# Optimization experiments

Measured on AMD Instinct MI355X. Metric: run time of the kernel, lower is better.

Reference implementation:

```python
import jax, jax.numpy as jnp
import numpy as np

NUM_NET = 2
V = 100000
D = 128
B = 4096
K = 5
NS = 10
HYP1 = 0.1
HYP2 = 0.1
HYP3 = 0.1


def setup_inputs() -> dict:
    key = jax.random.key(0)
    ks = jax.random.split(key, 10)
    ri = lambda k, shape: jax.random.randint(k, shape, 0, V, dtype=jnp.int32)
    return {
        "node_tables": jax.random.normal(ks[0], (NUM_NET, V, D), jnp.float32) * 0.1,
        "neigh_tables": jax.random.normal(ks[1], (NUM_NET, V, D), jnp.float32) * 0.1,
        "nodes_idx": ri(ks[2], (NUM_NET, B)),
        "neigh_idx": ri(ks[3], (NUM_NET, B, K)),
        "role_idx": ri(ks[4], (NUM_NET, NUM_NET, B)),
        "neg_main": ri(ks[5], (NUM_NET, B, K * NS)),
        "neg_node": ri(ks[6], (NUM_NET, NUM_NET, B, 1 * NS)),
        "neg_cross": ri(ks[7], (NUM_NET, NUM_NET, B, K * NS)),
        "neg_role": ri(ks[8], (NUM_NET, NUM_NET, B, 1 * NS)),
    }


def _pos_loss(ctx, node):
    # ctx: (B, M, D), node: (B, D) -> mean over all logsigmoid(ctx . node)
    return jax.nn.log_sigmoid(jnp.einsum("bmd,bd->bm", ctx, node)).mean()


def _neg_loss(neg_ctx, node):
    # ctx embeddings are negated: logsigmoid(-(neg . node)), sum over samples, mean over batch
    return jax.nn.log_sigmoid(-jnp.einsum("bmd,bd->bm", neg_ctx, node)).sum(axis=1).mean()


def reference(node_tables, neigh_tables, nodes_idx, neigh_idx, role_idx,
              neg_main, neg_node, neg_cross, neg_role):
    cost = []
    for i in range(NUM_NET):
        node_emb = node_tables[i][nodes_idx[i]]          # (B, D)
        # main SGNS loss on view i (neigh tables)
        neigh_emb = neigh_tables[i][neigh_idx[i]]        # (B, K, D)
        c = _pos_loss(neigh_emb, node_emb) + _neg_loss(neigh_tables[i][neg_main[i]], node_emb)
        cost.append(c)
        # cross-view node alignment (node tables of j at same node indices)
        for j in range(NUM_NET):
            if j != i:
                ctx = node_tables[j][nodes_idx[i]][:, None, :]   # (B, 1, D)
                c = _pos_loss(ctx, node_emb) + _neg_loss(node_tables[j][neg_node[i, j]], node_emb)
                cost.append(HYP1 * c)
        # cross-view neighbor loss (neigh tables of j at view-i neighbor indices)
        for j in range(NUM_NET):
            if j != i:
                ctx = neigh_tables[j][neigh_idx[i]]              # (B, K, D)
                c = _pos_loss(ctx, node_emb) + _neg_loss(neigh_tables[j][neg_cross[i, j]], node_emb)
                cost.append(HYP2 * c)
        # role-based loss (node tables of all j at role indices)
        for j in range(NUM_NET):
            ctx = node_tables[j][role_idx[i, j]][:, None, :]     # (B, 1, D)
            c = _pos_loss(ctx, node_emb) + _neg_loss(node_tables[j][neg_role[i, j]], node_emb)
            cost.append(HYP3 * c)
    total = cost[0]
    for c in cost[1:]:
        total = total + c
    return -total / len(cost)
```

## Files before the change

kernel.cpp:

```cpp
#include <hip/hip_runtime.h>

#define NUM_NET 2
#define V 100000
#define D 128
#define B 4096
#define K 5
#define NS 10

#define W_MAIN_POS (1.0f/20480.0f)
#define W_INV_B    (1.0f/4096.0f)
#define HYP_B      (0.1f/4096.0f)
#define HYP2_BK    (0.1f/20480.0f)

#define GLOBAL_AS __attribute__((address_space(1)))
#define LDS_AS    __attribute__((address_space(3)))

__device__ __forceinline__ void gl_lds16(const float* g, float* l) {
    __builtin_amdgcn_global_load_lds((const GLOBAL_AS unsigned int*)g,
                                     (LDS_AS unsigned int*)l, 16, 0, 0);
}

__device__ __forceinline__ float dot8(float4 a0, float4 a1, float4 b0, float4 b1) {
    return a0.x*b0.x + a0.y*b0.y + a0.z*b0.z + a0.w*b0.w
         + a1.x*b1.x + a1.y*b1.y + a1.z*b1.z + a1.w*b1.w;
}

__device__ __forceinline__ float wlogsig(float pp, int code) {
    float mag = (code == 0) ? W_MAIN_POS
              : (code == 3) ? W_INV_B
              : (code == 6) ? HYP2_BK
              : (code == 7) ? 0.0f
              : HYP_B;
    float x  = (code & 1) ? -pp : pp;
    float ls = fminf(x, 0.0f) - __logf(1.0f + __expf(-fabsf(x)));
    return mag * ls;
}

__global__ __launch_bounds__(256) void rmne_main(
    const float* __restrict__ node_tables,
    const float* __restrict__ neigh_tables,
    const int*   __restrict__ nodes_idx,
    const int*   __restrict__ neigh_idx,
    const int*   __restrict__ role_idx,
    const int*   __restrict__ neg_main,
    const int*   __restrict__ neg_node,
    const int*   __restrict__ neg_cross,
    const int*   __restrict__ neg_role,
    float*       __restrict__ out)
{
    __shared__ float lbuf[4][2][1024];

    const int tid  = threadIdx.x;
    const int lane = tid & 63;
    const int wave = tid >> 6;
    const int unit = blockIdx.x * 4 + wave;
    const int i = unit >> 12;
    const int b = unit & (B - 1);
    const int j = 1 - i;

    int pk[3];
    #pragma unroll
    for (int s = 0; s < 3; ++s) {
        int d = lane + 64 * s;
        int idx = 0, tab = 0, code = 7;
        if      (d <   5) { idx = neigh_idx[(i*B + b)*K + d];              tab = 2 + i; code = 0; }
        else if (d <  55) { idx = neg_main[(i*B + b)*50 + (d-5)];          tab = 2 + i; code = 3; }
        else if (d <  56) { idx = nodes_idx[i*B + b];                      tab = j;     code = 4; }
        else if (d <  66) { idx = neg_node[((i*2+j)*B + b)*NS + (d-56)];   tab = j;     code = 5; }
        else if (d <  71) { idx = neigh_idx[(i*B + b)*K + (d-66)];         tab = 2 + j; code = 6; }
        else if (d < 121) { idx = neg_cross[((i*2+j)*B + b)*50 + (d-71)];  tab = 2 + j; code = 5; }
        else if (d < 122) { idx = role_idx[(i*2+0)*B + b];                 tab = 0;     code = 4; }
        else if (d < 132) { idx = neg_role[((i*2+0)*B + b)*NS + (d-122)];  tab = 0;     code = 5; }
        else if (d < 133) { idx = role_idx[(i*2+1)*B + b];                 tab = 1;     code = 4; }
        else if (d < 143) { idx = neg_role[((i*2+1)*B + b)*NS + (d-133)];  tab = 1;     code = 5; }
        pk[s] = idx | (tab << 20) | (code << 22);
    }

    const int l16     = lane & 15;
    const int quarter = lane >> 4;
    const int nrow    = nodes_idx[i*B + b];
    const float4* nep = (const float4*)(node_tables + ((size_t)i*V + (size_t)nrow)*D) + l16*2;
    const float4 ne0 = nep[0];
    const float4 ne1 = nep[1];

    float acc = 0.0f;

    auto issue = [&](int bb, int parity) {
        float* Lb = &lbuf[wave][parity][0];
        #pragma unroll
        for (int t = 0; t < 4; ++t) {
            int e = 8*bb + 2*t + (lane >> 5);
            int p = __shfl(pk[bb >> 3], e & 63, 64);
            int idx = p & 0xFFFFF;
            int tab = (p >> 20) & 3;
            const float* base = (tab & 2) ? neigh_tables : node_tables;
            const float* g = base + ((size_t)(tab & 1)*V + (size_t)idx)*D + (lane & 31)*4;
            gl_lds16(g, Lb + t*256);
        }
    };

    auto compute = [&](int bb, int parity) {
        const float* Lb = &lbuf[wave][parity][0];
        #pragma unroll
        for (int it = 0; it < 2; ++it) {
            int ein = 4*it + quarter;
            int p = __shfl(pk[bb >> 3], (8*bb + ein) & 63, 64);
            const float4* r = (const float4*)(Lb + ein*128 + l16*8);
            float4 c0 = r[0];
            float4 c1 = r[1];
            float pp = dot8(ne0, ne1, c0, c1);
            pp += __shfl_xor(pp, 1, 64);
            pp += __shfl_xor(pp, 2, 64);
            pp += __shfl_xor(pp, 4, 64);
            pp += __shfl_xor(pp, 8, 64);
            acc += wlogsig(pp, (p >> 22) & 7);
        }
    };

    issue(0, 0);
    #pragma unroll
    for (int bb = 0; bb < 17; ++bb) {
        issue(bb + 1, (bb + 1) & 1);
        asm volatile("s_waitcnt vmcnt(4)" ::: "memory");
        compute(bb, bb & 1);
    }
    asm volatile("s_waitcnt vmcnt(0)" ::: "memory");
    compute(17, 1);

    acc += __shfl_xor(acc, 16, 64);
    acc += __shfl_xor(acc, 32, 64);

    __shared__ float wsum[4];
    if (lane == 0) wsum[wave] = acc;
    __syncthreads();
    if (tid == 0) {
        float s = wsum[0] + wsum[1] + wsum[2] + wsum[3];
        atomicAdd(out, s * (-1.0f / 10.0f));
    }
}

extern "C" void kernel_launch(void* const* d_in, const int* in_sizes, int n_in,
                              void* d_out, int out_size, void* d_ws, size_t ws_size,
                              hipStream_t stream) {
    const float* node_tables  = (const float*)d_in[0];
    const float* neigh_tables = (const float*)d_in[1];
    const int*   nodes_idx    = (const int*)d_in[2];
    const int*   neigh_idx    = (const int*)d_in[3];
    const int*   role_idx     = (const int*)d_in[4];
    const int*   neg_main     = (const int*)d_in[5];
    const int*   neg_node     = (const int*)d_in[6];
    const int*   neg_cross    = (const int*)d_in[7];
    const int*   neg_role     = (const int*)d_in[8];
    float* out = (float*)d_out;

    hipMemsetAsync(out, 0, sizeof(float), stream);
    rmne_main<<<2048, 256, 0, stream>>>(node_tables, neigh_tables, nodes_idx, neigh_idx,
                                        role_idx, neg_main, neg_node, neg_cross, neg_role, out);
}
```

Before: 295.3 us.

## Replace LDS async gather pipeline with register-prefetched direct row loads

Drops the global_load_lds double-buffered staging through shared memory. Each 16-lane quarter now loads its gathered row slice straight into registers through a three-deep rotating prefetch, with 4 rows per step. This removes the LDS writes and reads and the manual vmcnt waits. In exchange it issues extra padded loads past the real row count (weight-zero and tail prefetches), leaves fewer rows in flight per wave, and uses more registers.

```diff
diff --git a/kernel.cpp b/kernel.cpp
--- a/kernel.cpp
+++ b/kernel.cpp
@@ -11,14 +11,6 @@
 #define W_INV_B    (1.0f/4096.0f)
 #define HYP_B      (0.1f/4096.0f)
 #define HYP2_BK    (0.1f/20480.0f)
-
-#define GLOBAL_AS __attribute__((address_space(1)))
-#define LDS_AS    __attribute__((address_space(3)))
-
-__device__ __forceinline__ void gl_lds16(const float* g, float* l) {
-    __builtin_amdgcn_global_load_lds((const GLOBAL_AS unsigned int*)g,
-                                     (LDS_AS unsigned int*)l, 16, 0, 0);
-}
 
 __device__ __forceinline__ float dot8(float4 a0, float4 a1, float4 b0, float4 b1) {
     return a0.x*b0.x + a0.y*b0.y + a0.z*b0.z + a0.w*b0.w
@@ -48,8 +40,6 @@
     const int*   __restrict__ neg_role,
     float*       __restrict__ out)
 {
-    __shared__ float lbuf[4][2][1024];
-
     const int tid  = threadIdx.x;
     const int lane = tid & 63;
     const int wave = tid >> 6;
@@ -75,6 +65,7 @@
         else if (d < 143) { idx = neg_role[((i*2+1)*B + b)*NS + (d-133)];  tab = 1;     code = 5; }
         pk[s] = idx | (tab << 20) | (code << 22);
     }
+    const int pkv0 = pk[0], pkv1 = pk[1], pkv2 = pk[2];
 
     const int l16     = lane & 15;
     const int quarter = lane >> 4;
@@ -85,47 +76,41 @@
 
     float acc = 0.0f;
 
-    auto issue = [&](int bb, int parity) {
-        float* Lb = &lbuf[wave][parity][0];
-        #pragma unroll
-        for (int t = 0; t < 4; ++t) {
-            int e = 8*bb + 2*t + (lane >> 5);
-            int p = __shfl(pk[bb >> 3], e & 63, 64);
-            int idx = p & 0xFFFFF;
-            int tab = (p >> 20) & 3;
-            const float* base = (tab & 2) ? neigh_tables : node_tables;
-            const float* g = base + ((size_t)(tab & 1)*V + (size_t)idx)*D + (lane & 31)*4;
-            gl_lds16(g, Lb + t*256);
-        }
+    auto gete = [&](int tt) -> int {
+        int pks = (tt < 16) ? pkv0 : (tt < 32) ? pkv1 : pkv2;
+        return __shfl(pks, (4*tt + quarter) & 63, 64);
+    };
+    auto loadrow = [&](int e, float4& r0, float4& r1) {
+        int idx = e & 0xFFFFF;
+        int tab = (e >> 20) & 3;
+        const float* base = (tab & 2) ? neigh_tables : node_tables;
+        const float4* row = (const float4*)(base + ((size_t)(tab & 1)*V + (size_t)idx)*D) + l16*2;
+        r0 = row[0];
+        r1 = row[1];
+    };
+    auto stepf = [&](int tt, float4& r0, float4& r1, int& e) {
+        float pp = dot8(ne0, ne1, r0, r1);
+        pp += __shfl_xor(pp, 1, 64);
+        pp += __shfl_xor(pp, 2, 64);
+        pp += __shfl_xor(pp, 4, 64);
+        pp += __shfl_xor(pp, 8, 64);
+        acc += wlogsig(pp, (e >> 22) & 7);
+        e = gete(tt + 3);
+        loadrow(e, r0, r1);
     };
 
-    auto compute = [&](int bb, int parity) {
-        const float* Lb = &lbuf[wave][parity][0];
-        #pragma unroll
-        for (int it = 0; it < 2; ++it) {
-            int ein = 4*it + quarter;
-            int p = __shfl(pk[bb >> 3], (8*bb + ein) & 63, 64);
-            const float4* r = (const float4*)(Lb + ein*128 + l16*8);
-            float4 c0 = r[0];
-            float4 c1 = r[1];
-            float pp = dot8(ne0, ne1, c0, c1);
-            pp += __shfl_xor(pp, 1, 64);
-            pp += __shfl_xor(pp, 2, 64);
-            pp += __shfl_xor(pp, 4, 64);
-            pp += __shfl_xor(pp, 8, 64);
-            acc += wlogsig(pp, (p >> 22) & 7);
-        }
-    };
+    int e0 = gete(0), e1 = gete(1), e2 = gete(2);
+    float4 a0, a1, b0, b1, c0, c1;
+    loadrow(e0, a0, a1);
+    loadrow(e1, b0, b1);
+    loadrow(e2, c0, c1);
 
-    issue(0, 0);
     #pragma unroll
-    for (int bb = 0; bb < 17; ++bb) {
-        issue(bb + 1, (bb + 1) & 1);
-        asm volatile("s_waitcnt vmcnt(4)" ::: "memory");
-        compute(bb, bb & 1);
+    for (int t = 0; t < 39; t += 3) {
+        stepf(t,     a0, a1, e0);
+        stepf(t + 1, b0, b1, e1);
+        stepf(t + 2, c0, c1, e2);
     }
-    asm volatile("s_waitcnt vmcnt(0)" ::: "memory");
-    compute(17, 1);
 
     acc += __shfl_xor(acc, 16, 64);
     acc += __shfl_xor(acc, 32, 64);
```

New measurement: 276.7 us. 1.07x faster.
